# Optimization experiments

Hardware: AMD Instinct MI355X
Metric: run time of the kernel (lower is better)

The kernel has to match this reference:

```python
import jax, jax.numpy as jnp
import numpy as np

EMBED_DIM = 256
NUM_HEADS = 8
HEAD_DIM = EMBED_DIM // NUM_HEADS
CPB_HIDDEN = 64


def setup_inputs() -> dict:
    key = jax.random.key(0)
    ks = jax.random.split(key, 12)
    B, Q, K = 4, 900, 1024
    s = 0.02
    return {
        "nodes": jax.random.normal(ks[0], (B, Q, EMBED_DIM), jnp.float32),
        "images_data": jax.random.normal(ks[1], (B, K, EMBED_DIM), jnp.float32),
        "images_mask": jnp.zeros((B, K), dtype=bool),
        "relative_distances": jax.random.normal(ks[2], (B, Q, K, 2), jnp.float32),
        "Wq": jax.random.normal(ks[3], (EMBED_DIM, EMBED_DIM), jnp.float32) * s,
        "bq": jnp.zeros((EMBED_DIM,), jnp.float32),
        "Wkv": jax.random.normal(ks[4], (2 * EMBED_DIM, EMBED_DIM), jnp.float32) * s,
        "bkv": jnp.zeros((2 * EMBED_DIM,), jnp.float32),
        "Wc1": jax.random.normal(ks[5], (CPB_HIDDEN, 2), jnp.float32) * 0.5,
        "bc1": jnp.zeros((CPB_HIDDEN,), jnp.float32),
        "Wc2": jax.random.normal(ks[6], (NUM_HEADS, CPB_HIDDEN), jnp.float32) * 0.1,
        "bc2": jnp.zeros((NUM_HEADS,), jnp.float32),
        "Wo": jax.random.normal(ks[7], (EMBED_DIM, EMBED_DIM), jnp.float32) * s,
        "bo": jnp.zeros((EMBED_DIM,), jnp.float32),
    }


def reference(nodes, images_data, images_mask, relative_distances,
              Wq, bq, Wkv, bkv, Wc1, bc1, Wc2, bc2, Wo, bo):
    B, Q, K, _ = relative_distances.shape
    H, D = NUM_HEADS, HEAD_DIM

    # query / key / value projections
    q = nodes @ Wq.T + bq                       # [B, Q, E]
    q = q.reshape(B, Q, H, D).transpose(0, 2, 1, 3)  # [B, H, Q, D]
    kv = images_data @ Wkv.T + bkv              # [B, K, 2E]
    kv = kv.reshape(B, K, 2, H, D).transpose(2, 0, 3, 1, 4)  # [2, B, H, K, D]
    k, v = kv[0], kv[1]

    # continuous position bias MLP: [B,Q,K,2] -> [B,Q,K,H]
    h = jax.nn.relu(relative_distances @ Wc1.T + bc1)
    cpb = h @ Wc2.T + bc2                       # [B, Q, K, H]
    cpb = cpb.transpose(0, 3, 1, 2)             # [B, H, Q, K]

    # mask out padded image positions
    att_mask = jnp.where(images_mask[:, None, None, :], -jnp.inf, cpb)

    # scaled dot-product attention with additive mask
    scale = 1.0 / jnp.sqrt(jnp.asarray(D, q.dtype))
    scores = jnp.einsum("bhqd,bhkd->bhqk", q, k) * scale + att_mask
    attn = jax.nn.softmax(scores, axis=-1)
    out = jnp.einsum("bhqk,bhkd->bhqd", attn, v)  # [B, H, Q, D]

    out = out.transpose(0, 2, 1, 3).reshape(B, Q, H * D)
    return out @ Wo.T + bo
```

## Files before the change

kernel.cpp:

```cpp
#include <hip/hip_runtime.h>
#include <hip/hip_bf16.h>

typedef float f32x4 __attribute__((ext_vector_type(4)));
typedef short short8 __attribute__((ext_vector_type(8)));

static __device__ __forceinline__ short f2bf(float x) {
  union { __hip_bfloat16 b; short s; } u;
  u.b = __float2bfloat16(x);
  return u.s;
}

__global__ __launch_bounds__(256)
void cvt_bf16(const float* __restrict__ nodes, const float* __restrict__ images,
              const float* __restrict__ Wq, const float* __restrict__ Wkv,
              const float* __restrict__ Wo,
              short* __restrict__ nb, short* __restrict__ ib,
              short* __restrict__ wqb, short* __restrict__ wkvb,
              short* __restrict__ wob) {
  const int idx = blockIdx.x * 256 + threadIdx.x;
  const float* src; short* dst; int o;
  if      (idx < 115200) { src = nodes;  dst = nb;   o = idx; }
  else if (idx < 246272) { src = images; dst = ib;   o = idx - 115200; }
  else if (idx < 254464) { src = Wq;     dst = wqb;  o = idx - 246272; }
  else if (idx < 270848) { src = Wkv;    dst = wkvb; o = idx - 254464; }
  else                   { src = Wo;     dst = wob;  o = idx - 270848; }
  const float4 a = ((const float4*)src)[o * 2];
  const float4 b = ((const float4*)src)[o * 2 + 1];
  short8 v;
  v[0] = f2bf(a.x); v[1] = f2bf(a.y); v[2] = f2bf(a.z); v[3] = f2bf(a.w);
  v[4] = f2bf(b.x); v[5] = f2bf(b.y); v[6] = f2bf(b.z); v[7] = f2bf(b.w);
  *(short8*)&dst[o * 8] = v;
}

__global__ __launch_bounds__(256, 4)
void gemm_qkv_mfma(const short* __restrict__ nb, const short* __restrict__ wqb,
                   const float* __restrict__ bq, short* __restrict__ qb,
                   const short* __restrict__ ib, const short* __restrict__ wkvb,
                   const float* __restrict__ bkv, short* __restrict__ kb,
                   short* __restrict__ vT) {
  const int t = threadIdx.x, w = t >> 6, lane = t & 63;
  const int fr = lane & 15, fk = lane >> 4;
  int bid = blockIdx.x;
  const short *A, *W; const float* bias; int M, m0, n0, kvmode;
  if (bid < 228) {
    A = nb; W = wqb; bias = bq; M = 3600; kvmode = 0;
    m0 = (bid >> 2) * 64; n0 = (bid & 3) * 64;
  } else {
    bid -= 228;
    A = ib; W = wkvb; bias = bkv; M = 4096; kvmode = 1;
    m0 = (bid >> 3) * 64; n0 = (bid & 7) * 64;
  }
  int arow = m0 + w * 16 + fr; if (arow > M - 1) arow = M - 1;
  f32x4 acc[4];
  #pragma unroll
  for (int s = 0; s < 4; ++s) acc[s] = (f32x4){0.f, 0.f, 0.f, 0.f};
  #pragma unroll 2
  for (int k0 = 0; k0 < 256; k0 += 32) {
    const short8 af = *(const short8*)&A[(size_t)arow * 256 + k0 + fk * 8];
    #pragma unroll
    for (int s = 0; s < 4; ++s) {
      const short8 wf =
          *(const short8*)&W[(size_t)(n0 + s * 16 + fr) * 256 + k0 + fk * 8];
      acc[s] = __builtin_amdgcn_mfma_f32_16x16x32_bf16(af, wf, acc[s], 0, 0, 0);
    }
  }
  #pragma unroll
  for (int s = 0; s < 4; ++s)
    #pragma unroll
    for (int r = 0; r < 4; ++r) {
      const int m = m0 + w * 16 + fk * 4 + r;
      const int n = n0 + s * 16 + fr;
      const float val = acc[s][r] + bias[n];
      if (kvmode == 0) {
        if (m < 3600) qb[(size_t)m * 256 + n] = f2bf(val);
      } else {
        if (n < 256)
          kb[(size_t)m * 256 + n] = f2bf(val);
        else
          vT[((size_t)(m >> 10) * 256 + (n - 256)) * 1024 + (m & 1023)] =
              f2bf(val);
      }
    }
}

template <int NS>
__global__ __launch_bounds__(256, 4)
void gemm_out_combine(const float* __restrict__ Opart,
                      const float* __restrict__ msplit,
                      const float* __restrict__ lsplit,
                      const short* __restrict__ wob, const float* __restrict__ bo,
                      float* __restrict__ out) {
  const int t = threadIdx.x, w = t >> 6, lane = t & 63;
  const int fr = lane & 15, fk = lane >> 4;
  const int m0 = (blockIdx.x >> 2) * 64, n0 = (blockIdx.x & 3) * 64;
  int arow = m0 + w * 16 + fr; if (arow > 3599) arow = 3599;
  const int b = arow / 900, q = arow - b * 900;
  const int row912 = b * 912 + q;
  f32x4 acc[4];
  #pragma unroll
  for (int s = 0; s < 4; ++s) acc[s] = (f32x4){0.f, 0.f, 0.f, 0.f};
  #pragma unroll 2
  for (int k0 = 0; k0 < 256; k0 += 32) {
    const int h = k0 >> 5;
    float mv[NS], M = -1e30f;
    #pragma unroll
    for (int s = 0; s < NS; ++s) {
      mv[s] = msplit[((s * 4 + b) * 8 + h) * 912 + q];
      M = fmaxf(M, mv[s]);
    }
    float L = 0.f, wgt[NS];
    #pragma unroll
    for (int s = 0; s < NS; ++s) {
      wgt[s] = __expf(mv[s] - M);
      L = fmaf(lsplit[((s * 4 + b) * 8 + h) * 912 + q], wgt[s], L);
    }
    const float rL = 1.f / L;
    float av[8];
    #pragma unroll
    for (int j = 0; j < 8; ++j) av[j] = 0.f;
    #pragma unroll
    for (int s = 0; s < NS; ++s) {
      const float* op = &Opart[((size_t)s * 3648 + row912) * 256 + k0 + fk * 8];
      const float4 o0 = *(const float4*)op;
      const float4 o1 = *(const float4*)(op + 4);
      const float ws = wgt[s] * rL;
      av[0] = fmaf(o0.x, ws, av[0]); av[1] = fmaf(o0.y, ws, av[1]);
      av[2] = fmaf(o0.z, ws, av[2]); av[3] = fmaf(o0.w, ws, av[3]);
      av[4] = fmaf(o1.x, ws, av[4]); av[5] = fmaf(o1.y, ws, av[5]);
      av[6] = fmaf(o1.z, ws, av[6]); av[7] = fmaf(o1.w, ws, av[7]);
    }
    short8 af;
    #pragma unroll
    for (int j = 0; j < 8; ++j) af[j] = f2bf(av[j]);
    #pragma unroll
    for (int s = 0; s < 4; ++s) {
      const short8 wf =
          *(const short8*)&wob[(size_t)(n0 + s * 16 + fr) * 256 + k0 + fk * 8];
      acc[s] = __builtin_amdgcn_mfma_f32_16x16x32_bf16(af, wf, acc[s], 0, 0, 0);
    }
  }
  #pragma unroll
  for (int s = 0; s < 4; ++s)
    #pragma unroll
    for (int r = 0; r < 4; ++r) {
      const int m = m0 + w * 16 + fk * 4 + r;
      const int n = n0 + s * 16 + fr;
      if (m < 3600) out[(size_t)m * 256 + n] = acc[s][r] + bo[n];
    }
}

#define SCALE 0.17677669529663687f

#define BAR()                                              \
  asm volatile("s_waitcnt lgkmcnt(0)" ::: "memory");       \
  __builtin_amdgcn_s_barrier();                            \
  asm volatile("" ::: "memory")

template <int KLEN>
__global__ __launch_bounds__(512, 2)
void attn_part(const __hip_bfloat16* __restrict__ qb,
               const __hip_bfloat16* __restrict__ kb,
               const __hip_bfloat16* __restrict__ vT,
               const float* __restrict__ dist,
               const unsigned char* __restrict__ mask,
               const float* __restrict__ Wc1, const float* __restrict__ bc1,
               const float* __restrict__ Wc2, const float* __restrict__ bc2,
               float* __restrict__ Opart,
               float* __restrict__ msplit,
               float* __restrict__ lsplit) {
  constexpr int NCH = KLEN / 32;
  __shared__ float cpb_s[2][8 * 552];
  __shared__ short ps_s[8][640];

  const int t    = threadIdx.x;
  const int b    = blockIdx.x / 57;
  const int q0   = (blockIdx.x % 57) * 16;
  const int sp   = blockIdx.y;
  const int kb0  = sp * KLEN;
  const int w    = t >> 6;
  const int lane = t & 63;
  const int fr   = lane & 15;
  const int fk   = lane >> 4;

  float w1x[2][8], w1y[2][8], w1b[2][8];
  #pragma unroll
  for (int m = 0; m < 2; ++m)
    #pragma unroll
    for (int jj = 0; jj < 8; ++jj) {
      const int j = m * 32 + fk * 8 + jj;
      w1x[m][jj] = Wc1[2 * j];
      w1y[m][jj] = Wc1[2 * j + 1];
      w1b[m][jj] = bc1[j];
    }
  short8 w2f[2];
  #pragma unroll
  for (int m = 0; m < 2; ++m)
    #pragma unroll
    for (int jj = 0; jj < 8; ++jj) {
      const float v = (fr < 8) ? Wc2[fr * 64 + m * 32 + fk * 8 + jj] : 0.f;
      w2f[m][jj] = f2bf(v);
    }
  const float b2add = (fr < 8) ? bc2[fr] : 0.f;

  int qrow = q0 + fr; if (qrow > 899) qrow = 899;
  const short8 aq = *(const short8*)&qb[(size_t)(b * 900 + qrow) * 256 +
                                        w * 32 + fk * 8];

  const float* dptr[4];
  float2 d2cur[4];
  #pragma unroll
  for (int t4 = 0; t4 < 4; ++t4) {
    int qg = q0 + 2 * w + (t4 >> 1); if (qg > 899) qg = 899;
    dptr[t4] = dist +
        ((size_t)(b * 900 + qg) * 1024 + kb0 + (t4 & 1) * 16 + fr) * 2;
    d2cur[t4] = *(const float2*)dptr[t4];
  }

  f32x4 of[2];
  of[0] = (f32x4){0.f, 0.f, 0.f, 0.f};
  of[1] = (f32x4){0.f, 0.f, 0.f, 0.f};
  float mreg[4], lreg[4];
  #pragma unroll
  for (int r = 0; r < 4; ++r) { mreg[r] = -1e30f; lreg[r] = 0.f; }

  for (int c = 0; c < NCH; ++c) {
    const int k0 = kb0 + c * 32;
    const int cn = (c < NCH - 1) ? c + 1 : c;
    float* cpb_c = cpb_s[c & 1];

    float2 d2n[4];
    #pragma unroll
    for (int t4 = 0; t4 < 4; ++t4)
      d2n[t4] = *(const float2*)(dptr[t4] + (size_t)cn * 64);
    const short8 kf0 = *(const short8*)
        &kb[(size_t)(b * 1024 + k0 + fr) * 256 + w * 32 + fk * 8];
    const short8 kf1 = *(const short8*)
        &kb[(size_t)(b * 1024 + k0 + 16 + fr) * 256 + w * 32 + fk * 8];
    const short8 bv0 = *(const short8*)
        &vT[(size_t)(b * 256 + w * 32 + fr) * 1024 + k0 + fk * 8];
    const short8 bv1 = *(const short8*)
        &vT[(size_t)(b * 256 + w * 32 + 16 + fr) * 1024 + k0 + fk * 8];
    const bool mk0 = mask[b * 1024 + k0 + fr] != 0;
    const bool mk1 = mask[b * 1024 + k0 + 16 + fr] != 0;

    #pragma unroll
    for (int t4 = 0; t4 < 4; ++t4) {
      const float dx = d2cur[t4].x, dy = d2cur[t4].y;
      short8 a0, a1;
      #pragma unroll
      for (int jj = 0; jj < 8; ++jj) {
        const float h0 =
            fmaxf(fmaf(w1x[0][jj], dx, fmaf(w1y[0][jj], dy, w1b[0][jj])), 0.f);
        const float h1 =
            fmaxf(fmaf(w1x[1][jj], dx, fmaf(w1y[1][jj], dy, w1b[1][jj])), 0.f);
        a0[jj] = f2bf(h0);
        a1[jj] = f2bf(h1);
      }
      f32x4 z = {0.f, 0.f, 0.f, 0.f};
      f32x4 dcp = __builtin_amdgcn_mfma_f32_16x16x32_bf16(a1, w2f[1], z, 0, 0, 0);
      dcp = __builtin_amdgcn_mfma_f32_16x16x32_bf16(a0, w2f[0], dcp, 0, 0, 0);
      const int qloc = 2 * w + (t4 >> 1);
      const int kbase = (t4 & 1) * 16;
      if (fr < 8) {
        #pragma unroll
        for (int rr = 0; rr < 4; ++rr)
          cpb_c[fr * 552 + qloc * 34 + kbase + fk * 4 + rr] = dcp[rr] + b2add;
      }
      __builtin_amdgcn_sched_barrier(0);
    }

    BAR();

    f32x4 z = {0.f, 0.f, 0.f, 0.f};
    __builtin_amdgcn_s_setprio(1);
    const f32x4 sc0 = __builtin_amdgcn_mfma_f32_16x16x32_bf16(aq, kf0, z, 0, 0, 0);
    const f32x4 sc1 = __builtin_amdgcn_mfma_f32_16x16x32_bf16(aq, kf1, z, 0, 0, 0);
    __builtin_amdgcn_s_setprio(0);

    float s0v[4], s1v[4];
    bool need = false;
    #pragma unroll
    for (int r = 0; r < 4; ++r) {
      const int q = fk * 4 + r;
      const float cv0 = cpb_c[w * 552 + q * 34 + fr];
      const float cv1 = cpb_c[w * 552 + q * 34 + 16 + fr];
      s0v[r] = mk0 ? -1e30f : fmaf(sc0[r], SCALE, cv0);
      s1v[r] = mk1 ? -1e30f : fmaf(sc1[r], SCALE, cv1);
      need = need || (fmaxf(s0v[r], s1v[r]) > mreg[r] + 8.f);
    }
    if (__any((int)need)) {
      #pragma unroll
      for (int r = 0; r < 4; ++r) {
        float mx = fmaxf(s0v[r], s1v[r]);
        mx = fmaxf(mx, __shfl_xor(mx, 1));
        mx = fmaxf(mx, __shfl_xor(mx, 2));
        mx = fmaxf(mx, __shfl_xor(mx, 4));
        mx = fmaxf(mx, __shfl_xor(mx, 8));
        const float mnew = fmaxf(mreg[r], mx);
        const float al = __expf(mreg[r] - mnew);
        of[0][r] *= al;
        of[1][r] *= al;
        lreg[r] *= al;
        mreg[r] = mnew;
      }
    }
    #pragma unroll
    for (int r = 0; r < 4; ++r) {
      const int q = fk * 4 + r;
      const float p0 = __expf(s0v[r] - mreg[r]);
      const float p1 = __expf(s1v[r] - mreg[r]);
      ps_s[w][q * 40 + fr]      = f2bf(p0);
      ps_s[w][q * 40 + 16 + fr] = f2bf(p1);
      lreg[r] += p0 + p1;
    }

    asm volatile("s_waitcnt lgkmcnt(0)" ::: "memory");
    __builtin_amdgcn_sched_barrier(0);

    const short8 ap = *(const short8*)&ps_s[w][fr * 40 + fk * 8];
    __builtin_amdgcn_s_setprio(1);
    of[0] = __builtin_amdgcn_mfma_f32_16x16x32_bf16(ap, bv0, of[0], 0, 0, 0);
    of[1] = __builtin_amdgcn_mfma_f32_16x16x32_bf16(ap, bv1, of[1], 0, 0, 0);
    __builtin_amdgcn_s_setprio(0);

    #pragma unroll
    for (int t4 = 0; t4 < 4; ++t4) d2cur[t4] = d2n[t4];
  }

  #pragma unroll
  for (int r = 0; r < 4; ++r) {
    lreg[r] += __shfl_xor(lreg[r], 1);
    lreg[r] += __shfl_xor(lreg[r], 2);
    lreg[r] += __shfl_xor(lreg[r], 4);
    lreg[r] += __shfl_xor(lreg[r], 8);
  }

  #pragma unroll
  for (int s = 0; s < 2; ++s)
    #pragma unroll
    for (int r = 0; r < 4; ++r) {
      const int qg = q0 + fk * 4 + r;
      Opart[((size_t)sp * 3648 + b * 912 + qg) * 256 + w * 32 + s * 16 + fr] =
          of[s][r];
    }
  if (fr == 0) {
    #pragma unroll
    for (int r = 0; r < 4; ++r) {
      const int qg = q0 + fk * 4 + r;
      msplit[((sp * 4 + b) * 8 + w) * 912 + qg] = mreg[r];
      lsplit[((sp * 4 + b) * 8 + w) * 912 + qg] = lreg[r];
    }
  }
}

extern "C" void kernel_launch(void* const* d_in, const int* in_sizes, int n_in,
                              void* d_out, int out_size, void* d_ws, size_t ws_size,
                              hipStream_t stream) {
  const float* nodes  = (const float*)d_in[0];
  const float* images = (const float*)d_in[1];
  const unsigned char* mask = (const unsigned char*)d_in[2];
  const float* dist   = (const float*)d_in[3];
  const float* Wq     = (const float*)d_in[4];
  const float* bq     = (const float*)d_in[5];
  const float* Wkv    = (const float*)d_in[6];
  const float* bkv    = (const float*)d_in[7];
  const float* Wc1    = (const float*)d_in[8];
  const float* bc1    = (const float*)d_in[9];
  const float* Wc2    = (const float*)d_in[10];
  const float* bc2    = (const float*)d_in[11];
  const float* Wo     = (const float*)d_in[12];
  const float* bo     = (const float*)d_in[13];
  float* out = (float*)d_out;

  char* wp = (char*)d_ws;
  short* qb = (short*)wp;
  short* kb = (short*)(wp + 1843200);
  short* vT = (short*)(wp + 3940352);
  char*  S  = wp + 6037504;
  short* nb   = (short*)S;
  short* ib   = (short*)(S + 1843200);
  short* wqb  = (short*)(S + 3940352);
  short* wkvb = (short*)(S + 4071424);
  float* Opart = (float*)S;

  const size_t need2 = 6037504u + 7938048u + 131072u;
  int nsplit = (ws_size >= need2) ? 2 : 1;
  const size_t Ssize = (nsplit == 2)
      ? 7938048u
      : 4333568u;
  short* wob = (short*)(S + Ssize);
  float* msplit = Opart + (size_t)nsplit * 3648 * 256;
  float* lsplit = msplit + (size_t)nsplit * 4 * 8 * 912;

  cvt_bf16<<<1090, 256, 0, stream>>>(nodes, images, Wq, Wkv, Wo,
                                     nb, ib, wqb, wkvb, wob);
  gemm_qkv_mfma<<<740, 256, 0, stream>>>(nb, wqb, bq, qb, ib, wkvb, bkv, kb, vT);

  if (nsplit == 2) {
    attn_part<512><<<dim3(228, 2), 512, 0, stream>>>(
        (const __hip_bfloat16*)qb, (const __hip_bfloat16*)kb,
        (const __hip_bfloat16*)vT, dist, mask, Wc1, bc1, Wc2, bc2,
        Opart, msplit, lsplit);
    gemm_out_combine<2><<<228, 256, 0, stream>>>(Opart, msplit, lsplit,
                                                 wob, bo, out);
  } else {
    attn_part<1024><<<dim3(228, 1), 512, 0, stream>>>(
        (const __hip_bfloat16*)qb, (const __hip_bfloat16*)kb,
        (const __hip_bfloat16*)vT, dist, mask, Wc1, bc1, Wc2, bc2,
        Opart, msplit, lsplit);
    gemm_out_combine<1><<<228, 256, 0, stream>>>(Opart, msplit, lsplit,
                                                 wob, bo, out);
  }
}
```

Before: 117.5 us.

## Add 4-way key split for attention and store position bias in bf16 LDS

Adds a four-way split of the key dimension when the workspace is large enough, launching 912 attention blocks instead of 456 and combining the partial results in the output GEMM. It also stores the position-bias tile in LDS as bf16 instead of fp32, halving its shared-memory footprint, which may help occupancy. The extra split raises partial-output traffic and combine work. The bf16 bias adds rounding error to the scores.

```diff
diff --git a/kernel.cpp b/kernel.cpp
--- a/kernel.cpp
+++ b/kernel.cpp
@@ -8,6 +8,11 @@
   union { __hip_bfloat16 b; short s; } u;
   u.b = __float2bfloat16(x);
   return u.s;
+}
+static __device__ __forceinline__ float bf2f(short s) {
+  union { unsigned u; float f; } x;
+  x.u = ((unsigned)(unsigned short)s) << 16;
+  return x.f;
 }
 
 __global__ __launch_bounds__(256)
@@ -169,7 +174,7 @@
                float* __restrict__ msplit,
                float* __restrict__ lsplit) {
   constexpr int NCH = KLEN / 32;
-  __shared__ float cpb_s[2][8 * 552];
+  __shared__ short cpb_s[2][8 * 552];
   __shared__ short ps_s[8][640];
 
   const int t    = threadIdx.x;
@@ -226,7 +231,7 @@
   for (int c = 0; c < NCH; ++c) {
     const int k0 = kb0 + c * 32;
     const int cn = (c < NCH - 1) ? c + 1 : c;
-    float* cpb_c = cpb_s[c & 1];
+    short* cpb_c = cpb_s[c & 1];
 
     float2 d2n[4];
     #pragma unroll
@@ -264,7 +269,8 @@
       if (fr < 8) {
         #pragma unroll
         for (int rr = 0; rr < 4; ++rr)
-          cpb_c[fr * 552 + qloc * 34 + kbase + fk * 4 + rr] = dcp[rr] + b2add;
+          cpb_c[fr * 552 + qloc * 34 + kbase + fk * 4 + rr] =
+              f2bf(dcp[rr] + b2add);
       }
       __builtin_amdgcn_sched_barrier(0);
     }
@@ -282,8 +288,8 @@
     #pragma unroll
     for (int r = 0; r < 4; ++r) {
       const int q = fk * 4 + r;
-      const float cv0 = cpb_c[w * 552 + q * 34 + fr];
-      const float cv1 = cpb_c[w * 552 + q * 34 + 16 + fr];
+      const float cv0 = bf2f(cpb_c[w * 552 + q * 34 + fr]);
+      const float cv1 = bf2f(cpb_c[w * 552 + q * 34 + 16 + fr]);
       s0v[r] = mk0 ? -1e30f : fmaf(sc0[r], SCALE, cv0);
       s1v[r] = mk1 ? -1e30f : fmaf(sc1[r], SCALE, cv1);
       need = need || (fmaxf(s0v[r], s1v[r]) > mreg[r] + 8.f);
@@ -383,12 +389,17 @@
   short* wkvb = (short*)(S + 4071424);
   float* Opart = (float*)S;
 
-  const size_t need2 = 6037504u + 7938048u + 131072u;
-  int nsplit = (ws_size >= need2) ? 2 : 1;
-  const size_t Ssize = (nsplit == 2)
-      ? 7938048u
-      : 4333568u;
-  short* wob = (short*)(S + Ssize);
+  const size_t opart_b  = (size_t)3648 * 256 * 4;
+  const size_t ml_b     = (size_t)4 * 8 * 912 * 4;
+  const size_t need4 = 6037504u + 4 * (opart_b + 2 * ml_b) + 131072u;
+  const size_t need2 = 6037504u + 2 * (opart_b + 2 * ml_b) + 131072u;
+  int nsplit = 1;
+  if (ws_size >= need4) nsplit = 4;
+  else if (ws_size >= need2) nsplit = 2;
+  const size_t Ssize = (nsplit == 4) ? 4 * (opart_b + 2 * ml_b)
+                     : (nsplit == 2) ? 2 * (opart_b + 2 * ml_b)
+                                     : 4333568u;
+  short* wob = (short*)(S + ((Ssize > 4333568u) ? Ssize : 4333568u));
   float* msplit = Opart + (size_t)nsplit * 3648 * 256;
   float* lsplit = msplit + (size_t)nsplit * 4 * 8 * 912;
 
@@ -396,7 +407,14 @@
                                      nb, ib, wqb, wkvb, wob);
   gemm_qkv_mfma<<<740, 256, 0, stream>>>(nb, wqb, bq, qb, ib, wkvb, bkv, kb, vT);
 
-  if (nsplit == 2) {
+  if (nsplit == 4) {
+    attn_part<256><<<dim3(228, 4), 512, 0, stream>>>(
+        (const __hip_bfloat16*)qb, (const __hip_bfloat16*)kb,
+        (const __hip_bfloat16*)vT, dist, mask, Wc1, bc1, Wc2, bc2,
+        Opart, msplit, lsplit);
+    gemm_out_combine<4><<<228, 256, 0, stream>>>(Opart, msplit, lsplit,
+                                                 wob, bo, out);
+  } else if (nsplit == 2) {
     attn_part<512><<<dim3(228, 2), 512, 0, stream>>>(
         (const __hip_bfloat16*)qb, (const __hip_bfloat16*)kb,
         (const __hip_bfloat16*)vT, dist, mask, Wc1, bc1, Wc2, bc2,
```

Result: slower. 133.6 us (+13.8%).
